# Performance work log

Measured on AMD Instinct MI355X. Metric: run time of the kernel, lower is better.

The kernel has to match this reference:

```python
import jax, jax.numpy as jnp
import numpy as np

FEATS = 1024
HEAD = 16
MLP_HIDDEN = 4096
B, N = 8, 1024
EPS = 1e-5


def _layernorm(x, g, b):
    mu = jnp.mean(x, axis=-1, keepdims=True)
    var = jnp.var(x, axis=-1, keepdims=True)
    return (x - mu) * jax.lax.rsqrt(var + EPS) * g + b


def setup_inputs() -> dict:
    key = jax.random.key(0)
    ks = jax.random.split(key, 12)
    s_attn = 1.0 / np.sqrt(FEATS)
    s_mlp1 = 1.0 / np.sqrt(FEATS)
    s_mlp2 = 1.0 / np.sqrt(MLP_HIDDEN)
    return {
        "x": jax.random.normal(ks[0], (B, N, FEATS), dtype=jnp.float32),
        "ln1_g": jnp.ones((FEATS,), jnp.float32),
        "ln1_b": jnp.zeros((FEATS,), jnp.float32),
        "wq": jax.random.normal(ks[1], (FEATS, FEATS), jnp.float32) * s_attn,
        "bq": jnp.zeros((FEATS,), jnp.float32),
        "wk": jax.random.normal(ks[2], (FEATS, FEATS), jnp.float32) * s_attn,
        "bk": jnp.zeros((FEATS,), jnp.float32),
        "wv": jax.random.normal(ks[3], (FEATS, FEATS), jnp.float32) * s_attn,
        "bv": jnp.zeros((FEATS,), jnp.float32),
        "wo": jax.random.normal(ks[4], (FEATS, FEATS), jnp.float32) * s_attn,
        "bo": jnp.zeros((FEATS,), jnp.float32),
        "ln2_g": jnp.ones((FEATS,), jnp.float32),
        "ln2_b": jnp.zeros((FEATS,), jnp.float32),
        "w1": jax.random.normal(ks[5], (FEATS, MLP_HIDDEN), jnp.float32) * s_mlp1,
        "b1": jnp.zeros((MLP_HIDDEN,), jnp.float32),
        "w2": jax.random.normal(ks[6], (MLP_HIDDEN, FEATS), jnp.float32) * s_mlp2,
        "b2": jnp.zeros((FEATS,), jnp.float32),
    }


def reference(x, ln1_g, ln1_b, wq, bq, wk, bk, wv, bv, wo, bo,
              ln2_g, ln2_b, w1, b1, w2, b2):
    b, n, f = x.shape
    d = f // HEAD
    sqrt_d = jnp.asarray(f, x.dtype) ** 0.5  # NOTE: scale by sqrt(feats), as in source

    h = _layernorm(x, ln1_g, ln1_b)
    # [b, n, f] -> [b, head, n, d]
    q = (h @ wq + bq).reshape(b, n, HEAD, d).transpose(0, 2, 1, 3)
    k = (h @ wk + bk).reshape(b, n, HEAD, d).transpose(0, 2, 1, 3)
    v = (h @ wv + bv).reshape(b, n, HEAD, d).transpose(0, 2, 1, 3)

    score = jnp.einsum('bhif,bhjf->bhij', q, k) / sqrt_d
    p = jax.nn.softmax(score, axis=-1)
    attn = jnp.einsum('bhij,bhjf->bihf', p, v).reshape(b, n, f)
    o = attn @ wo + bo
    out = o + x

    h2 = _layernorm(out, ln2_g, ln2_b)
    m = jax.nn.gelu(h2 @ w1 + b1, approximate=False)
    m = jax.nn.gelu(m @ w2 + b2, approximate=False)
    return m + out
```

## Files before the change

kernel.cpp:

```cpp
#include <hip/hip_runtime.h>
#include <cstdint>

typedef __bf16 bf16;
typedef __attribute__((ext_vector_type(8))) __bf16 bf16x8;
typedef __attribute__((ext_vector_type(4))) __bf16 bf16x4;
typedef __attribute__((ext_vector_type(4))) float f32x4;
typedef __attribute__((ext_vector_type(8))) unsigned short u16x8;

#define AS1C(p) ((const __attribute__((address_space(1))) void*)(p))
#define AS3(p)  ((__attribute__((address_space(3))) void*)(p))

__device__ __forceinline__ float gelu_exact(float v) {
    return 0.5f * v * (1.0f + erff(v * 0.7071067811865476f));
}

__global__ __launch_bounds__(256, 1) void wtrans_kernel(
    const float* __restrict__ w, bf16* __restrict__ wt, int K, int N)
{
    __shared__ float tile[64][65];
    const int k0 = blockIdx.y * 64, n0 = blockIdx.x * 64;
    const int tid = threadIdx.x;
    {
        const int kl = tid >> 2, nc = (tid & 3) * 16;
        #pragma unroll
        for (int i = 0; i < 4; ++i) {
            const float4 v = *(const float4*)&w[(size_t)(k0 + kl) * N + n0 + nc + i * 4];
            tile[kl][nc + i * 4 + 0] = v.x;
            tile[kl][nc + i * 4 + 1] = v.y;
            tile[kl][nc + i * 4 + 2] = v.z;
            tile[kl][nc + i * 4 + 3] = v.w;
        }
    }
    __syncthreads();
    {
        const int nl = tid >> 2, kc = (tid & 3) * 16;
        #pragma unroll
        for (int i = 0; i < 4; ++i) {
            bf16x4 o4;
            o4[0] = (bf16)tile[kc + i * 4 + 0][nl];
            o4[1] = (bf16)tile[kc + i * 4 + 1][nl];
            o4[2] = (bf16)tile[kc + i * 4 + 2][nl];
            o4[3] = (bf16)tile[kc + i * 4 + 3][nl];
            *(bf16x4*)&wt[(size_t)(n0 + nl) * K + k0 + kc + i * 4] = o4;
        }
    }
}

__global__ void bias3_kernel(const float* __restrict__ a, const float* __restrict__ b,
                             const float* __restrict__ c, float* __restrict__ o)
{
    const int i = blockIdx.x * 256 + threadIdx.x;
    o[i] = (i < 1024) ? a[i] : (i < 2048 ? b[i - 1024] : c[i - 2048]);
}

__global__ __launch_bounds__(256, 1) void ln_kernel(
    const float* __restrict__ x, const float* __restrict__ gw,
    const float* __restrict__ bw, bf16* __restrict__ out)
{
    const int row = blockIdx.x, tid = threadIdx.x;
    const float4 v = *(const float4*)&x[(size_t)row * 1024 + tid * 4];
    float s = v.x + v.y + v.z + v.w;
    float q = v.x * v.x + v.y * v.y + v.z * v.z + v.w * v.w;
    #pragma unroll
    for (int off = 32; off > 0; off >>= 1) {
        s += __shfl_xor(s, off);
        q += __shfl_xor(q, off);
    }
    __shared__ float red[8];
    if ((tid & 63) == 0) { red[tid >> 6] = s; red[4 + (tid >> 6)] = q; }
    __syncthreads();
    s = red[0] + red[1] + red[2] + red[3];
    q = red[4] + red[5] + red[6] + red[7];
    const float mu = s * (1.f / 1024.f);
    const float rs = rsqrtf(q * (1.f / 1024.f) - mu * mu + 1e-5f);
    const float4 gg = *(const float4*)&gw[tid * 4];
    const float4 bb = *(const float4*)&bw[tid * 4];
    bf16x4 o4;
    o4[0] = (bf16)((v.x - mu) * rs * gg.x + bb.x);
    o4[1] = (bf16)((v.y - mu) * rs * gg.y + bb.y);
    o4[2] = (bf16)((v.z - mu) * rs * gg.z + bb.z);
    o4[3] = (bf16)((v.w - mu) * rs * gg.w + bb.w);
    *(bf16x4*)&out[(size_t)row * 1024 + tid * 4] = o4;
}

template<int BCH>
__device__ __forceinline__ void stage_tile(
    const bf16* __restrict__ A, const bf16* __restrict__ BT, int K,
    int bm, int bn, int k0, char* buf, int wid, int rsub, int ksub)
{
    #pragma unroll
    for (int c = 0; c < 4; ++c) {
        const bf16* src = A + (size_t)(bm + c * 64 + wid * 8 + rsub) * K + k0 + ksub;
        __builtin_amdgcn_global_load_lds(AS1C(src), AS3(buf + (c * 8 + wid) * 1024), 16, 0, 0);
    }
    #pragma unroll
    for (int c = 0; c < BCH; ++c) {
        const bf16* src = BT + (size_t)(bn + c * 64 + wid * 8 + rsub) * K + k0 + ksub;
        __builtin_amdgcn_global_load_lds(AS1C(src), AS3(buf + 32768 + (c * 8 + wid) * 1024), 16, 0, 0);
    }
}

template<int EPI, int BN>
__global__ __launch_bounds__(512, 2) void gemm8p_kernel(
    const bf16* __restrict__ A, const bf16* __restrict__ BT,
    const float* __restrict__ bias, const float* __restrict__ res,
    void* __restrict__ out, int M, int N, int K)
{
    constexpr int PWM = (BN == 256) ? 128 : 64;
    constexpr int PWN = 64;
    constexpr int MF = PWM / 16;
    constexpr int NF = 4;
    constexpr int PH_M = (BN == 256) ? 4 : 2;
    constexpr int PH_N = (BN == 256) ? 2 : 4;
    constexpr int QN = NF / PH_N;
    constexpr int NPH = (MF / PH_M) * QN;
    constexpr int BCH = BN / 64;
    constexpr int BUFB = (256 + BN) * 128;
    constexpr int NBUF = (BN == 256) ? 2 : 3;
    extern __shared__ char lds[];

    const int tid = threadIdx.x;
    const int lane = tid & 63, wid = tid >> 6;
    const int wr = (BN == 256) ? (wid >> 2) : (wid >> 1);
    const int wc = (BN == 256) ? (wid & 3) : (wid & 1);
    const int j = lane & 15, g = lane >> 4;
    const int lanep = (lane & 7) ^ ((lane >> 4) & 3) ^ ((wid & 1) << 2);
    const int rsub = lane >> 3, ksub = lanep * 8;

    const int nbn = N / BN;
    const int nwg = (M / 256) * nbn;
    const int bid = blockIdx.x;
    const int wg = (bid & 7) * (nwg >> 3) + (bid >> 3);
    const int bm = (wg / nbn) * 256;
    const int bn = (wg % nbn) * BN;

    f32x4 acc[MF][NF] = {};
    const int NT = K >> 6;

    stage_tile<BCH>(A, BT, K, bm, bn, 0, lds, wid, rsub, ksub);
    if constexpr (NBUF == 3) {
        stage_tile<BCH>(A, BT, K, bm, bn, 64, lds + BUFB, wid, rsub, ksub);
        asm volatile("s_waitcnt vmcnt(6)" ::: "memory");
    } else {
        asm volatile("s_waitcnt vmcnt(0)" ::: "memory");
    }
    __builtin_amdgcn_s_barrier();

    for (int t = 0; t < NT; ++t) {
        char* buf = lds + ((NBUF == 2) ? (t & 1) : (t % 3)) * BUFB;
        #pragma unroll
        for (int ph = 0; ph < NPH; ++ph) {
            const int qm = ph / QN, qn = ph % QN;
            bf16x8 af[PH_M][2], bfr[PH_N][2];
            #pragma unroll
            for (int mf = 0; mf < PH_M; ++mf)
                #pragma unroll
                for (int ks = 0; ks < 2; ++ks) {
                    const int R = wr * PWM + (qm * PH_M + mf) * 16 + j;
                    uint32_t lb = (uint32_t)(R * 128 + ks * 64 + g * 16);
                    lb ^= (lb >> 4) & 0x70u;
                    af[mf][ks] = *(const bf16x8*)(buf + lb);
                }
            #pragma unroll
            for (int nf = 0; nf < PH_N; ++nf)
                #pragma unroll
                for (int ks = 0; ks < 2; ++ks) {
                    const int R = wc * PWN + (qn * PH_N + nf) * 16 + j;
                    uint32_t lb = (uint32_t)(R * 128 + ks * 64 + g * 16);
                    lb ^= (lb >> 4) & 0x70u;
                    bfr[nf][ks] = *(const bf16x8*)(buf + 32768 + lb);
                }
            if (ph == 0) {
                if constexpr (NBUF == 2) {
                    if (t + 1 < NT)
                        stage_tile<BCH>(A, BT, K, bm, bn, (t + 1) << 6,
                                        lds + ((t + 1) & 1) * BUFB, wid, rsub, ksub);
                } else {
                    if (t + 2 < NT)
                        stage_tile<BCH>(A, BT, K, bm, bn, (t + 2) << 6,
                                        lds + ((t + 2) % 3) * BUFB, wid, rsub, ksub);
                }
            }
            __builtin_amdgcn_s_barrier();
            asm volatile("s_waitcnt lgkmcnt(0)" ::: "memory");
            __builtin_amdgcn_sched_barrier(0);
            __builtin_amdgcn_s_setprio(1);
            #pragma unroll
            for (int mf = 0; mf < PH_M; ++mf)
                #pragma unroll
                for (int nf = 0; nf < PH_N; ++nf)
                    #pragma unroll
                    for (int ks = 0; ks < 2; ++ks)
                        acc[qm * PH_M + mf][qn * PH_N + nf] =
                            __builtin_amdgcn_mfma_f32_16x16x32_bf16(
                                af[mf][ks], bfr[nf][ks],
                                acc[qm * PH_M + mf][qn * PH_N + nf], 0, 0, 0);
            __builtin_amdgcn_s_setprio(0);
            if (ph == NPH - 1) {
                if constexpr (NBUF == 2) {
                    asm volatile("s_waitcnt vmcnt(0)" ::: "memory");
                } else {
                    if (t + 2 < NT) asm volatile("s_waitcnt vmcnt(6)" ::: "memory");
                    else            asm volatile("s_waitcnt vmcnt(0)" ::: "memory");
                }
            }
            __builtin_amdgcn_s_barrier();
        }
    }

    const int row0 = bm + wr * PWM;
    const int col0 = bn + wc * PWN;
    #pragma unroll
    for (int nf = 0; nf < NF; ++nf) {
        const int col = col0 + nf * 16 + j;
        const float bs = bias[col];
        #pragma unroll
        for (int mf = 0; mf < MF; ++mf) {
            #pragma unroll
            for (int r = 0; r < 4; ++r) {
                const int row = row0 + mf * 16 + g * 4 + r;
                float v = acc[mf][nf][r] + bs;
                if constexpr (EPI == 2 || EPI == 3) v = gelu_exact(v);
                if constexpr (EPI == 1 || EPI == 3) {
                    v += res[(size_t)row * N + col];
                    ((float*)out)[(size_t)row * N + col] = v;
                } else {
                    ((bf16*)out)[(size_t)row * N + col] = (bf16)v;
                }
            }
        }
    }
}

__device__ __forceinline__ void attn_iter(
    int c, const bf16* __restrict__ Kp, const bf16* __restrict__ Vp,
    uint32_t (&vTu)[2][64][36],
    bf16x8 (&kf)[4][2], bf16x8 (&kfn)[4][2],
    const bf16x8& qf0, const bf16x8& qf1,
    f32x4 (&o)[4], float& mrun, float& lsum,
    int kp, int d0, int jperm, int g, int j)
{
    const f32x4 zero = {0.f, 0.f, 0.f, 0.f};
    const bool pf = (c + 1 < 16);

    u16x8 r0, r1;
    if (pf) {
        const size_t vb = (size_t)((c + 1) * 64 + kp) * 3072 + d0;
        r0 = *(const u16x8*)&Vp[vb];
        r1 = *(const u16x8*)&Vp[vb + 3072];
    }

    f32x4 s[4];
    #pragma unroll
    for (int t = 0; t < 4; ++t) {
        s[t] = __builtin_amdgcn_mfma_f32_16x16x32_bf16(kf[t][0], qf0, zero, 0, 0, 0);
        s[t] = __builtin_amdgcn_mfma_f32_16x16x32_bf16(kf[t][1], qf1, s[t], 0, 0, 0);
    }

    if (pf) {
        #pragma unroll
        for (int t = 0; t < 4; ++t) {
            const int key = (c + 1) * 64 + (t >> 1) * 32 + jperm + (t & 1) * 4;
            kfn[t][0] = *(const bf16x8*)&Kp[(size_t)key * 3072 + g * 8];
            kfn[t][1] = *(const bf16x8*)&Kp[(size_t)key * 3072 + 32 + g * 8];
        }
    }

    float cur = fmaxf(fmaxf(s[0][0], s[0][1]), fmaxf(s[0][2], s[0][3]));
    #pragma unroll
    for (int t = 1; t < 4; ++t)
        cur = fmaxf(cur, fmaxf(fmaxf(s[t][0], s[t][1]), fmaxf(s[t][2], s[t][3])));
    cur = fmaxf(cur, __shfl_xor(cur, 16));
    cur = fmaxf(cur, __shfl_xor(cur, 32));

    if (!__all(cur - mrun <= 8.0f)) {
        const float mnew = fmaxf(mrun, cur);
        const float alpha = __expf(mrun - mnew);
        float al[4];
        #pragma unroll
        for (int r = 0; r < 4; ++r) al[r] = __shfl(alpha, g * 4 + r);
        #pragma unroll
        for (int dt = 0; dt < 4; ++dt)
            #pragma unroll
            for (int r = 0; r < 4; ++r) o[dt][r] *= al[r];
        lsum *= alpha;
        mrun = mnew;
    }
    float ps = 0.f;
    #pragma unroll
    for (int t = 0; t < 4; ++t)
        #pragma unroll
        for (int r = 0; r < 4; ++r) {
            const float p = __expf(s[t][r] - mrun);
            s[t][r] = p;
            ps += p;
        }
    lsum += ps;

    bf16x8 pa0, pa1;
    #pragma unroll
    for (int r = 0; r < 4; ++r) {
        pa0[r]     = (bf16)s[0][r];
        pa0[4 + r] = (bf16)s[1][r];
        pa1[r]     = (bf16)s[2][r];
        pa1[4 + r] = (bf16)s[3][r];
    }

    if (pf) {
        #pragma unroll
        for (int i = 0; i < 8; ++i)
            vTu[(c + 1) & 1][d0 + i][kp >> 1] = (uint32_t)r0[i] | ((uint32_t)r1[i] << 16);
    }

    #pragma unroll
    for (int dt = 0; dt < 4; ++dt) {
        const bf16* vrow = (const bf16*)&vTu[c & 1][dt * 16 + j][0];
        const bf16x8 vb0 = *(const bf16x8*)(vrow + g * 8);
        const bf16x8 vb1 = *(const bf16x8*)(vrow + 32 + g * 8);
        o[dt] = __builtin_amdgcn_mfma_f32_16x16x32_bf16(pa0, vb0, o[dt], 0, 0, 0);
        o[dt] = __builtin_amdgcn_mfma_f32_16x16x32_bf16(pa1, vb1, o[dt], 0, 0, 0);
    }
    __syncthreads();
}

__global__ __launch_bounds__(256, 1) void attn_kernel(
    const bf16* __restrict__ qkv, bf16* __restrict__ attn)
{
    const int tid = threadIdx.x;
    const int lane = tid & 63, wid = tid >> 6;
    const int j = lane & 15, g = lane >> 4;

    const int lin = blockIdx.x + blockIdx.y * 16;
    const int virt = (lin & 7) * 256 + (lin >> 3);
    const int bh = virt >> 4, qt = virt & 15;
    const int b = bh >> 4, h = bh & 15;
    const int q0 = qt * 64 + wid * 16;

    const bf16* Qp = qkv + (size_t)b * 1024 * 3072 + h * 64;
    const bf16* Kp = Qp + 1024;
    const bf16* Vp = Qp + 2048;

    __shared__ __attribute__((aligned(16))) uint32_t vTu[2][64][36];

    const int kp = (tid & 31) * 2;
    const int d0 = (tid >> 5) * 8;
    {
        const u16x8 r0 = *(const u16x8*)&Vp[(size_t)kp * 3072 + d0];
        const u16x8 r1 = *(const u16x8*)&Vp[(size_t)(kp + 1) * 3072 + d0];
        #pragma unroll
        for (int i = 0; i < 8; ++i)
            vTu[0][d0 + i][kp >> 1] = (uint32_t)r0[i] | ((uint32_t)r1[i] << 16);
    }

    bf16x8 qf0 = *(const bf16x8*)&Qp[(size_t)(q0 + j) * 3072 + g * 8];
    bf16x8 qf1 = *(const bf16x8*)&Qp[(size_t)(q0 + j) * 3072 + 32 + g * 8];
    #pragma unroll
    for (int e = 0; e < 8; ++e) {
        qf0[e] = (bf16)((float)qf0[e] * 0.03125f);
        qf1[e] = (bf16)((float)qf1[e] * 0.03125f);
    }

    const int jperm = (j >> 2) * 8 + (j & 3);

    f32x4 o[4] = {};
    float mrun = -1e30f, lsum = 0.f;

    bf16x8 kfA[4][2], kfB[4][2];
    #pragma unroll
    for (int t = 0; t < 4; ++t) {
        const int key = (t >> 1) * 32 + jperm + (t & 1) * 4;
        kfA[t][0] = *(const bf16x8*)&Kp[(size_t)key * 3072 + g * 8];
        kfA[t][1] = *(const bf16x8*)&Kp[(size_t)key * 3072 + 32 + g * 8];
    }

    __syncthreads();

    for (int cc = 0; cc < 16; cc += 2) {
        attn_iter(cc,     Kp, Vp, vTu, kfA, kfB, qf0, qf1, o, mrun, lsum, kp, d0, jperm, g, j);
        attn_iter(cc + 1, Kp, Vp, vTu, kfB, kfA, qf0, qf1, o, mrun, lsum, kp, d0, jperm, g, j);
    }

    lsum += __shfl_xor(lsum, 16);
    lsum += __shfl_xor(lsum, 32);
    float inv[4];
    #pragma unroll
    for (int r = 0; r < 4; ++r) inv[r] = 1.0f / __shfl(lsum, g * 4 + r);
    #pragma unroll
    for (int dt = 0; dt < 4; ++dt)
        #pragma unroll
        for (int r = 0; r < 4; ++r)
            attn[(size_t)(b * 1024 + q0 + g * 4 + r) * 1024 + h * 64 + dt * 16 + j] =
                (bf16)(o[dt][r] * inv[r]);
}

extern "C" void kernel_launch(void* const* d_in, const int* in_sizes, int n_in,
                              void* d_out, int out_size, void* d_ws, size_t ws_size,
                              hipStream_t stream)
{
    const float* x    = (const float*)d_in[0];
    const float* ln1g = (const float*)d_in[1];
    const float* ln1b = (const float*)d_in[2];
    const float* wq   = (const float*)d_in[3];
    const float* bq   = (const float*)d_in[4];
    const float* wk   = (const float*)d_in[5];
    const float* bk   = (const float*)d_in[6];
    const float* wv   = (const float*)d_in[7];
    const float* bv   = (const float*)d_in[8];
    const float* wo   = (const float*)d_in[9];
    const float* bo   = (const float*)d_in[10];
    const float* ln2g = (const float*)d_in[11];
    const float* ln2b = (const float*)d_in[12];
    const float* w1   = (const float*)d_in[13];
    const float* b1   = (const float*)d_in[14];
    const float* w2   = (const float*)d_in[15];
    const float* b2   = (const float*)d_in[16];

    char* ws = (char*)d_ws;
    bf16* wqkvT = (bf16*)ws;  ws += (size_t)3072 * 1024 * 2;
    bf16* woT   = (bf16*)ws;  ws += (size_t)1024 * 1024 * 2;
    bf16* w1T   = (bf16*)ws;  ws += (size_t)4096 * 1024 * 2;
    bf16* w2T   = (bf16*)ws;  ws += (size_t)1024 * 4096 * 2;
    float* bqkv = (float*)ws; ws += (size_t)3072 * 4;
    bf16* h     = (bf16*)ws;  ws += (size_t)8192 * 1024 * 2;
    bf16* qkv   = (bf16*)ws;  ws += (size_t)8192 * 3072 * 2;
    bf16* attn  = (bf16*)ws;  ws += (size_t)8192 * 1024 * 2;
    float* outf = (float*)ws; ws += (size_t)8192 * 1024 * 4;
    bf16* m1    = (bf16*)ws;  ws += (size_t)8192 * 4096 * 2;

    (void)hipFuncSetAttribute((const void*)gemm8p_kernel<0, 128>,
                              hipFuncAttributeMaxDynamicSharedMemorySize, 147456);
    (void)hipFuncSetAttribute((const void*)gemm8p_kernel<1, 128>,
                              hipFuncAttributeMaxDynamicSharedMemorySize, 147456);
    (void)hipFuncSetAttribute((const void*)gemm8p_kernel<2, 256>,
                              hipFuncAttributeMaxDynamicSharedMemorySize, 131072);
    (void)hipFuncSetAttribute((const void*)gemm8p_kernel<3, 128>,
                              hipFuncAttributeMaxDynamicSharedMemorySize, 147456);

    wtrans_kernel<<<dim3(16, 16), 256, 0, stream>>>(wq, wqkvT,                   1024, 1024);
    wtrans_kernel<<<dim3(16, 16), 256, 0, stream>>>(wk, wqkvT + 1024 * 1024,     1024, 1024);
    wtrans_kernel<<<dim3(16, 16), 256, 0, stream>>>(wv, wqkvT + 2 * 1024 * 1024, 1024, 1024);
    wtrans_kernel<<<dim3(16, 16), 256, 0, stream>>>(wo, woT, 1024, 1024);
    wtrans_kernel<<<dim3(64, 16), 256, 0, stream>>>(w1, w1T, 1024, 4096);
    wtrans_kernel<<<dim3(16, 64), 256, 0, stream>>>(w2, w2T, 4096, 1024);
    bias3_kernel<<<12, 256, 0, stream>>>(bq, bk, bv, bqkv);

    ln_kernel<<<8192, 256, 0, stream>>>(x, ln1g, ln1b, h);
    gemm8p_kernel<0, 128><<<768, 512, 147456, stream>>>(h, wqkvT, bqkv, nullptr, qkv, 8192, 3072, 1024);
    attn_kernel<<<dim3(16, 128), 256, 0, stream>>>(qkv, attn);
    gemm8p_kernel<1, 128><<<256, 512, 147456, stream>>>(attn, woT, bo, x, outf, 8192, 1024, 1024);
    ln_kernel<<<8192, 256, 0, stream>>>(outf, ln2g, ln2b, h);
    gemm8p_kernel<2, 256><<<512, 512, 131072, stream>>>(h, w1T, b1, nullptr, m1, 8192, 4096, 1024);
    gemm8p_kernel<3, 128><<<256, 512, 147456, stream>>>(m1, w2T, b2, outf, (float*)d_out, 8192, 1024, 4096);
}
```

Baseline: 553.2 us.

## Replace GEMM with 256-wide N tiles and per-phase staggered global-to-LDS loads

Replaces the GEMM kernel with one that uses a fixed 256-column B tile and a configurable M tile of 256 rows with 8 waves or 128 rows with 4 waves. Each wave computes a 128x64 sub-tile split across two N halves. Global-to-LDS staging for the next K tile is now spread over the four compute phases in a fixed group order, with matching vmcnt waits, instead of being issued all at once. QKV, out-proj and MLP2 now use the new shapes: the N=1024 GEMMs get 256-thread blocks with smaller LDS, and QKV moves from 768 to 384 blocks. The attention launch is split into two half-grids by batch-head range, which adds a launch without changing the work.

```diff
diff --git a/kernel.cpp b/kernel.cpp
--- a/kernel.cpp
+++ b/kernel.cpp
@@ -83,102 +83,95 @@
     *(bf16x4*)&out[(size_t)row * 1024 + tid * 4] = o4;
 }
 
-template<int BCH>
-__device__ __forceinline__ void stage_tile(
-    const bf16* __restrict__ A, const bf16* __restrict__ BT, int K,
-    int bm, int bn, int k0, char* buf, int wid, int rsub, int ksub)
-{
-    #pragma unroll
-    for (int c = 0; c < 4; ++c) {
-        const bf16* src = A + (size_t)(bm + c * 64 + wid * 8 + rsub) * K + k0 + ksub;
-        __builtin_amdgcn_global_load_lds(AS1C(src), AS3(buf + (c * 8 + wid) * 1024), 16, 0, 0);
-    }
-    #pragma unroll
-    for (int c = 0; c < BCH; ++c) {
-        const bf16* src = BT + (size_t)(bn + c * 64 + wid * 8 + rsub) * K + k0 + ksub;
-        __builtin_amdgcn_global_load_lds(AS1C(src), AS3(buf + 32768 + (c * 8 + wid) * 1024), 16, 0, 0);
-    }
-}
-
-template<int EPI, int BN>
-__global__ __launch_bounds__(512, 2) void gemm8p_kernel(
+constexpr int GORD2[8]  = {0, 2, 16, 17, 18, 19, 1, 3};
+constexpr int GOFF2[5]  = {0, 4, 6, 8, 8};
+constexpr int GORD1[12] = {0, 1, 16, 17, 18, 19, 20, 21, 22, 23, 2, 3};
+constexpr int GOFF1[5]  = {0, 6, 10, 12, 12};
+
+template<int EPI, int WM>
+__global__ __launch_bounds__(WM * 256, 2) void gemm_m201_kernel(
     const bf16* __restrict__ A, const bf16* __restrict__ BT,
     const float* __restrict__ bias, const float* __restrict__ res,
     void* __restrict__ out, int M, int N, int K)
 {
-    constexpr int PWM = (BN == 256) ? 128 : 64;
-    constexpr int PWN = 64;
-    constexpr int MF = PWM / 16;
-    constexpr int NF = 4;
-    constexpr int PH_M = (BN == 256) ? 4 : 2;
-    constexpr int PH_N = (BN == 256) ? 2 : 4;
-    constexpr int QN = NF / PH_N;
-    constexpr int NPH = (MF / PH_M) * QN;
-    constexpr int BCH = BN / 64;
-    constexpr int BUFB = (256 + BN) * 128;
-    constexpr int NBUF = (BN == 256) ? 2 : 3;
+    constexpr int BM = WM * 128;
+    constexpr int THREADS = WM * 256;
+    constexpr int RPG = THREADS / 8;
+    constexpr int ABYTES = BM * 128;
+    constexpr int BUFB = ABYTES + 256 * 128;
+    constexpr int NSG = (WM == 2) ? 8 : 12;
     extern __shared__ char lds[];
 
     const int tid = threadIdx.x;
     const int lane = tid & 63, wid = tid >> 6;
-    const int wr = (BN == 256) ? (wid >> 2) : (wid >> 1);
-    const int wc = (BN == 256) ? (wid & 3) : (wid & 1);
+    const int wr = (WM == 2) ? (wid >> 2) : 0;
+    const int wc = wid & 3;
     const int j = lane & 15, g = lane >> 4;
     const int lanep = (lane & 7) ^ ((lane >> 4) & 3) ^ ((wid & 1) << 2);
-    const int rsub = lane >> 3, ksub = lanep * 8;
-
-    const int nbn = N / BN;
-    const int nwg = (M / 256) * nbn;
+    const int ksub = lanep * 8;
+
+    const int nbn = N >> 8;
+    const int nwg = (M / BM) * nbn;
     const int bid = blockIdx.x;
     const int wg = (bid & 7) * (nwg >> 3) + (bid >> 3);
-    const int bm = (wg / nbn) * 256;
-    const int bn = (wg % nbn) * BN;
-
-    f32x4 acc[MF][NF] = {};
+    const int bm = (wg / nbn) * BM;
+    const int bn = (wg % nbn) << 8;
+
+    auto stage_one = [&](int id, int k0, char* obuf) {
+        const int isB = id >> 4, gg = id & 15;
+        const bf16* base = isB ? BT : A;
+        const int rowbase = (isB ? bn : bm) + gg * RPG;
+        const bf16* src = base + (size_t)(rowbase + (tid >> 3)) * K + k0 + ksub;
+        char* dst = obuf + (isB ? ABYTES : 0) + gg * (RPG * 128) + wid * 1024;
+        __builtin_amdgcn_global_load_lds(AS1C(src), AS3(dst), 16, 0, 0);
+    };
+
+    f32x4 acc[8][4] = {};
     const int NT = K >> 6;
 
-    stage_tile<BCH>(A, BT, K, bm, bn, 0, lds, wid, rsub, ksub);
-    if constexpr (NBUF == 3) {
-        stage_tile<BCH>(A, BT, K, bm, bn, 64, lds + BUFB, wid, rsub, ksub);
-        asm volatile("s_waitcnt vmcnt(6)" ::: "memory");
-    } else {
-        asm volatile("s_waitcnt vmcnt(0)" ::: "memory");
-    }
+    #pragma unroll
+    for (int i = 0; i < NSG; ++i)
+        stage_one((WM == 2) ? GORD2[i] : GORD1[i], 0, lds);
+    if constexpr (WM == 2) asm volatile("s_waitcnt vmcnt(4)" ::: "memory");
+    else                   asm volatile("s_waitcnt vmcnt(6)" ::: "memory");
     __builtin_amdgcn_s_barrier();
 
     for (int t = 0; t < NT; ++t) {
-        char* buf = lds + ((NBUF == 2) ? (t & 1) : (t % 3)) * BUFB;
-        #pragma unroll
-        for (int ph = 0; ph < NPH; ++ph) {
-            const int qm = ph / QN, qn = ph % QN;
-            bf16x8 af[PH_M][2], bfr[PH_N][2];
+        char* buf  = lds + (t & 1) * BUFB;
+        char* obuf = lds + ((t + 1) & 1) * BUFB;
+        #pragma unroll
+        for (int ph = 0; ph < 4; ++ph) {
+            const int qm = ph >> 1, qn = ph & 1;
+            bf16x8 af[4][2], bfr[2][2];
             #pragma unroll
-            for (int mf = 0; mf < PH_M; ++mf)
+            for (int mf = 0; mf < 4; ++mf)
                 #pragma unroll
                 for (int ks = 0; ks < 2; ++ks) {
-                    const int R = wr * PWM + (qm * PH_M + mf) * 16 + j;
+                    const int R = wr * 128 + (qm * 4 + mf) * 16 + j;
                     uint32_t lb = (uint32_t)(R * 128 + ks * 64 + g * 16);
                     lb ^= (lb >> 4) & 0x70u;
                     af[mf][ks] = *(const bf16x8*)(buf + lb);
                 }
             #pragma unroll
-            for (int nf = 0; nf < PH_N; ++nf)
+            for (int nfi = 0; nfi < 2; ++nfi)
                 #pragma unroll
                 for (int ks = 0; ks < 2; ++ks) {
-                    const int R = wc * PWN + (qn * PH_N + nf) * 16 + j;
+                    const int R = qn * 128 + wc * 32 + nfi * 16 + j;
                     uint32_t lb = (uint32_t)(R * 128 + ks * 64 + g * 16);
                     lb ^= (lb >> 4) & 0x70u;
-                    bfr[nf][ks] = *(const bf16x8*)(buf + 32768 + lb);
+                    bfr[nfi][ks] = *(const bf16x8*)(buf + ABYTES + lb);
                 }
-            if (ph == 0) {
-                if constexpr (NBUF == 2) {
-                    if (t + 1 < NT)
-                        stage_tile<BCH>(A, BT, K, bm, bn, (t + 1) << 6,
-                                        lds + ((t + 1) & 1) * BUFB, wid, rsub, ksub);
+            if (t + 1 < NT) {
+                if constexpr (WM == 2) {
+                    #pragma unroll
+                    for (int i = 0; i < 8; ++i)
+                        if (i >= GOFF2[ph] && i < GOFF2[ph + 1])
+                            stage_one(GORD2[i], (t + 1) << 6, obuf);
                 } else {
-                    if (t + 2 < NT)
-                        stage_tile<BCH>(A, BT, K, bm, bn, (t + 2) << 6,
-                                        lds + ((t + 2) % 3) * BUFB, wid, rsub, ksub);
+                    #pragma unroll
+                    for (int i = 0; i < 12; ++i)
+                        if (i >= GOFF1[ph] && i < GOFF1[ph + 1])
+                            stage_one(GORD1[i], (t + 1) << 6, obuf);
                 }
             }
             __builtin_amdgcn_s_barrier();
@@ -186,36 +179,37 @@
             __builtin_amdgcn_sched_barrier(0);
             __builtin_amdgcn_s_setprio(1);
             #pragma unroll
-            for (int mf = 0; mf < PH_M; ++mf)
+            for (int mf = 0; mf < 4; ++mf)
                 #pragma unroll
-                for (int nf = 0; nf < PH_N; ++nf)
+                for (int nfi = 0; nfi < 2; ++nfi)
                     #pragma unroll
                     for (int ks = 0; ks < 2; ++ks)
-                        acc[qm * PH_M + mf][qn * PH_N + nf] =
+                        acc[qm * 4 + mf][qn * 2 + nfi] =
                             __builtin_amdgcn_mfma_f32_16x16x32_bf16(
-                                af[mf][ks], bfr[nf][ks],
-                                acc[qm * PH_M + mf][qn * PH_N + nf], 0, 0, 0);
+                                af[mf][ks], bfr[nfi][ks],
+                                acc[qm * 4 + mf][qn * 2 + nfi], 0, 0, 0);
             __builtin_amdgcn_s_setprio(0);
-            if (ph == NPH - 1) {
-                if constexpr (NBUF == 2) {
-                    asm volatile("s_waitcnt vmcnt(0)" ::: "memory");
-                } else {
-                    if (t + 2 < NT) asm volatile("s_waitcnt vmcnt(6)" ::: "memory");
-                    else            asm volatile("s_waitcnt vmcnt(0)" ::: "memory");
-                }
+            if constexpr (WM == 2) {
+                if (ph == 0 || ph == 1) asm volatile("s_waitcnt vmcnt(6)" ::: "memory");
+                else if (ph == 2)       asm volatile("s_waitcnt vmcnt(8)" ::: "memory");
+                else                    asm volatile("s_waitcnt vmcnt(4)" ::: "memory");
+            } else {
+                if (ph == 0)            asm volatile("s_waitcnt vmcnt(8)" ::: "memory");
+                else if (ph == 1)       asm volatile("s_waitcnt vmcnt(10)" ::: "memory");
+                else if (ph == 2)       asm volatile("s_waitcnt vmcnt(12)" ::: "memory");
+                else                    asm volatile("s_waitcnt vmcnt(6)" ::: "memory");
             }
             __builtin_amdgcn_s_barrier();
         }
     }
 
-    const int row0 = bm + wr * PWM;
-    const int col0 = bn + wc * PWN;
-    #pragma unroll
-    for (int nf = 0; nf < NF; ++nf) {
-        const int col = col0 + nf * 16 + j;
+    const int row0 = bm + wr * 128;
+    #pragma unroll
+    for (int nf = 0; nf < 4; ++nf) {
+        const int col = bn + (nf >> 1) * 128 + wc * 32 + (nf & 1) * 16 + j;
         const float bs = bias[col];
         #pragma unroll
-        for (int mf = 0; mf < MF; ++mf) {
+        for (int mf = 0; mf < 8; ++mf) {
             #pragma unroll
             for (int r = 0; r < 4; ++r) {
                 const int row = row0 + mf * 16 + g * 4 + r;
@@ -324,15 +318,15 @@
 }
 
 __global__ __launch_bounds__(256, 1) void attn_kernel(
-    const bf16* __restrict__ qkv, bf16* __restrict__ attn)
+    const bf16* __restrict__ qkv, bf16* __restrict__ attn, int bh_base)
 {
     const int tid = threadIdx.x;
     const int lane = tid & 63, wid = tid >> 6;
     const int j = lane & 15, g = lane >> 4;
 
     const int lin = blockIdx.x + blockIdx.y * 16;
-    const int virt = (lin & 7) * 256 + (lin >> 3);
-    const int bh = virt >> 4, qt = virt & 15;
+    const int virt = (lin & 7) * 128 + (lin >> 3);
+    const int bh = bh_base + (virt >> 4), qt = virt & 15;
     const int b = bh >> 4, h = bh & 15;
     const int q0 = qt * 64 + wid * 16;
 
@@ -427,14 +421,14 @@
     float* outf = (float*)ws; ws += (size_t)8192 * 1024 * 4;
     bf16* m1    = (bf16*)ws;  ws += (size_t)8192 * 4096 * 2;
 
-    (void)hipFuncSetAttribute((const void*)gemm8p_kernel<0, 128>,
-                              hipFuncAttributeMaxDynamicSharedMemorySize, 147456);
-    (void)hipFuncSetAttribute((const void*)gemm8p_kernel<1, 128>,
-                              hipFuncAttributeMaxDynamicSharedMemorySize, 147456);
-    (void)hipFuncSetAttribute((const void*)gemm8p_kernel<2, 256>,
+    (void)hipFuncSetAttribute((const void*)gemm_m201_kernel<0, 2>,
                               hipFuncAttributeMaxDynamicSharedMemorySize, 131072);
-    (void)hipFuncSetAttribute((const void*)gemm8p_kernel<3, 128>,
-                              hipFuncAttributeMaxDynamicSharedMemorySize, 147456);
+    (void)hipFuncSetAttribute((const void*)gemm_m201_kernel<2, 2>,
+                              hipFuncAttributeMaxDynamicSharedMemorySize, 131072);
+    (void)hipFuncSetAttribute((const void*)gemm_m201_kernel<1, 1>,
+                              hipFuncAttributeMaxDynamicSharedMemorySize, 98304);
+    (void)hipFuncSetAttribute((const void*)gemm_m201_kernel<3, 1>,
+                              hipFuncAttributeMaxDynamicSharedMemorySize, 98304);
 
     wtrans_kernel<<<dim3(16, 16), 256, 0, stream>>>(wq, wqkvT,                   1024, 1024);
     wtrans_kernel<<<dim3(16, 16), 256, 0, stream>>>(wk, wqkvT + 1024 * 1024,     1024, 1024);
@@ -445,10 +439,11 @@
     bias3_kernel<<<12, 256, 0, stream>>>(bq, bk, bv, bqkv);
 
     ln_kernel<<<8192, 256, 0, stream>>>(x, ln1g, ln1b, h);
-    gemm8p_kernel<0, 128><<<768, 512, 147456, stream>>>(h, wqkvT, bqkv, nullptr, qkv, 8192, 3072, 1024);
-    attn_kernel<<<dim3(16, 128), 256, 0, stream>>>(qkv, attn);
-    gemm8p_kernel<1, 128><<<256, 512, 147456, stream>>>(attn, woT, bo, x, outf, 8192, 1024, 1024);
+    gemm_m201_kernel<0, 2><<<384, 512, 131072, stream>>>(h, wqkvT, bqkv, nullptr, qkv, 8192, 3072, 1024);
+    attn_kernel<<<dim3(16, 64), 256, 0, stream>>>(qkv, attn, 0);
+    attn_kernel<<<dim3(16, 64), 256, 0, stream>>>(qkv, attn, 64);
+    gemm_m201_kernel<1, 1><<<256, 256, 98304, stream>>>(attn, woT, bo, x, outf, 8192, 1024, 1024);
     ln_kernel<<<8192, 256, 0, stream>>>(outf, ln2g, ln2b, h);
-    gemm8p_kernel<2, 256><<<512, 512, 131072, stream>>>(h, w1T, b1, nullptr, m1, 8192, 4096, 1024);
-    gemm8p_kernel<3, 128><<<256, 512, 147456, stream>>>(m1, w2T, b2, outf, (float*)d_out, 8192, 1024, 4096);
-}
+    gemm_m201_kernel<2, 2><<<512, 512, 131072, stream>>>(h, w1T, b1, nullptr, m1, 8192, 4096, 1024);
+    gemm_m201_kernel<3, 1><<<256, 256, 98304, stream>>>(m1, w2T, b2, outf, (float*)d_out, 8192, 1024, 4096);
+}
```

Result: faster. 540.3 us (-2.3%).
